# Kernel optimization log

Measured on AMD Instinct MI355X. Metric: run time of the kernel, lower is better.

Reference implementation:

```python
import jax, jax.numpy as jnp
import numpy as np

EPS = 1e-5
CIN = [3, 24, 48, 96, 192]
COUT = [24, 48, 96, 192, 384]
P = 512
NUM_CLASSES = 101
FC_IN = 384 * 16 * 3 * 3  # 55296


def _poly_layer(x, proj, alpha, gamma, beta):
    # x: (B, C, D, H, W)
    B, C, D, H, W = x.shape
    # im2col: 3x3x3 patches with zero padding 1 -> (B, C*27, D, H, W)
    patches = jax.lax.conv_general_dilated_patches(
        x, filter_shape=(3, 3, 3), window_strides=(1, 1, 1),
        padding=[(1, 1), (1, 1), (1, 1)])
    patches = jnp.moveaxis(patches, 1, -1)  # (B, D, H, W, C*27)
    ws = jnp.einsum('bdhwk,pk->bdhwp', patches, proj)      # projector GEMM
    out = jnp.einsum('bdhwp,po->bdhwo', ws, alpha)         # alpha GEMM
    out = jnp.maximum(1.0 + out, 0.0)                      # clamp(1+x, min=0)
    out = jnp.moveaxis(out, -1, 1)                         # (B, O, D, H, W)
    # MaxPool3d kernel/stride (1,2,2)
    out = jax.lax.reduce_window(out, -jnp.inf, jax.lax.max,
                                (1, 1, 1, 2, 2), (1, 1, 1, 2, 2), 'VALID')
    # BatchNorm3d with batch statistics (train-mode math)
    mean = out.mean(axis=(0, 2, 3, 4), keepdims=True)
    var = out.var(axis=(0, 2, 3, 4), keepdims=True)
    out = (out - mean) * jax.lax.rsqrt(var + EPS)
    out = out * gamma.reshape(1, -1, 1, 1, 1) + beta.reshape(1, -1, 1, 1, 1)
    return out


def setup_inputs() -> dict:
    key = jax.random.key(0)
    keys = jax.random.split(key, 32)
    inp = {'x': jax.random.normal(keys[0], (2, 3, 16, 112, 112), dtype=jnp.float32)}
    ki = 1
    for i in range(5):
        k_feat = CIN[i] * 27
        inp[f'p{i+1}'] = jax.random.normal(keys[ki], (P, k_feat), dtype=jnp.float32) / np.sqrt(k_feat); ki += 1
        inp[f'a{i+1}'] = jax.random.normal(keys[ki], (P, COUT[i]), dtype=jnp.float32) * np.sqrt(2.0 / COUT[i]); ki += 1
        inp[f'g{i+1}'] = jnp.ones((COUT[i],), dtype=jnp.float32)
        inp[f'q{i+1}'] = jnp.zeros((COUT[i],), dtype=jnp.float32)
    inp['w1'] = jax.random.normal(keys[ki], (512, FC_IN), dtype=jnp.float32) * np.sqrt(2.0 / 512); ki += 1
    inp['b1'] = jnp.zeros((512,), dtype=jnp.float32)
    inp['w2'] = jax.random.normal(keys[ki], (256, 512), dtype=jnp.float32) * np.sqrt(2.0 / 256); ki += 1
    inp['b2'] = jnp.zeros((256,), dtype=jnp.float32)
    inp['w3'] = jax.random.normal(keys[ki], (NUM_CLASSES, 256), dtype=jnp.float32) * np.sqrt(2.0 / NUM_CLASSES); ki += 1
    inp['b3'] = jnp.zeros((NUM_CLASSES,), dtype=jnp.float32)
    return inp


def reference(x, p1, a1, g1, q1, p2, a2, g2, q2, p3, a3, g3, q3,
              p4, a4, g4, q4, p5, a5, g5, q5, w1, b1, w2, b2, w3, b3):
    projs = [p1, p2, p3, p4, p5]
    alphas = [a1, a2, a3, a4, a5]
    gammas = [g1, g2, g3, g4, g5]
    betas = [q1, q2, q3, q4, q5]
    h = x
    for i in range(5):
        h = _poly_layer(h, projs[i], alphas[i], gammas[i], betas[i])
    h = h.reshape(h.shape[0], -1)  # (B, 55296)
    h = jax.nn.relu(h @ w1.T + b1)  # dropout = identity (eval)
    h = jax.nn.relu(h @ w2.T + b2)
    logits = h @ w3.T + b3
    return logits
```

## Files before the change

### kernel.cpp

```cpp
#include <hip/hip_runtime.h>

#define EPS_BN 1e-5f

typedef __attribute__((ext_vector_type(8))) short sh8;
typedef __attribute__((ext_vector_type(4))) short sh4;
typedef __attribute__((ext_vector_type(4))) float f32x4;

static const size_t PART_OFF = 2645784;
static const size_t PRE_OFF  = 6258456;
static const size_t OUT5_OFF = 8666904;
static const size_t H_OFF    = 8777496;
static const size_t ST_OFF   = 8888088;
static const size_t BNP_OFF  = 8888856;
static const size_t H1_OFF   = 8938008;
static const size_t WS_TOT   = 8939032;
__device__ __align__(256) float g_ws[WS_TOT];

static const size_t XIN_OFF = 0;
static const size_t A1_OFF  = 1871424;
static const size_t A2_OFF  = 4776768;
static const size_t A3_OFF  = 6331968;
static const size_t A4_OFF  = 7216704;
static const size_t AR_TOT  = 7776576;
__device__ __align__(256) unsigned short g_act[AR_TOT];

static const size_t WB_OFF[5] = {0, 4096, 36352, 162304, 659968};
static const size_t WB_TOT    = 2650624;
__device__ __align__(256) unsigned short g_wb[WB_TOT];

__device__ inline unsigned short f2bf(float v) {
    unsigned u = __float_as_uint(v);
    return (unsigned short)((u + 0x7fffu + ((u >> 16) & 1u)) >> 16);
}
__device__ inline float bf2f(unsigned short h) {
    return __uint_as_float(((unsigned)h) << 16);
}

__global__ __launch_bounds__(256) void init_input(const float* __restrict__ x,
                                                  unsigned short* __restrict__ xp,
                                                  float* __restrict__ bnp,
                                                  int4* __restrict__ zp, int nz,
                                                  int4* __restrict__ wbz, int nwb)
{
    const int i = blockIdx.x * 256 + threadIdx.x;
    if (i < nz) zp[i] = make_int4(0, 0, 0, 0);
    if (i < nwb) wbz[i] = make_int4(0, 0, 0, 0);
    if (i < 49152) bnp[i] = 0.f;
    if (i >= 2 * 18 * 114 * 114 * 4) return;
    const int c = i & 3;
    int t = i >> 2;
    const int xx = t % 114; t /= 114;
    const int yy = t % 114; t /= 114;
    const int zz = t % 18;
    const int b  = t / 18;
    float v = 0.f;
    if (c < 3 && (unsigned)(zz - 1) < 16u && (unsigned)(yy - 1) < 112u && (unsigned)(xx - 1) < 112u)
        v = x[(((size_t)b * 3 + c) * 16 + (zz - 1)) * 12544 + (yy - 1) * 112 + (xx - 1)];
    xp[i] = f2bf(v);
}

struct PrepArgs {
    const float* src[10];
    int W[10];
    int dstrow[10];
    int start[11];
    int rowtot;
};

__global__ __launch_bounds__(256) void prep_t(PrepArgs a, unsigned short* __restrict__ dst)
{
    __shared__ unsigned short tileh[32 * 72];
    __shared__ unsigned short tilel[32 * 72];
    int m = 0;
    {
        const int bx = blockIdx.x;
        while (m < 9 && bx >= a.start[m + 1]) ++m;
    }
    const int t  = blockIdx.x - a.start[m];
    const int tw = t >> 4, tp = t & 15;
    const int p0 = tp * 32, w0 = tw * 64;
    const int W = a.W[m];
    const float* __restrict__ src = a.src[m];
    const int tid = threadIdx.x;

    #pragma unroll
    for (int e = 0; e < 8; ++e) {
        const int idx = tid + e * 256;
        const int w = idx & 63, pr = idx >> 6;
        const int gw = w0 + w;
        float v = 0.f;
        if (gw < W) v = src[(size_t)(p0 + pr) * W + gw];
        const unsigned short hh = f2bf(v);
        tileh[pr * 72 + w] = hh;
        tilel[pr * 72 + w] = f2bf(v - bf2f(hh));
    }
    __syncthreads();
    {
        const int wr = tid >> 2, pg = (tid & 3) * 8;
        sh8 packh, packl;
        #pragma unroll
        for (int e = 0; e < 8; ++e) {
            packh[e] = (short)tileh[(pg + e) * 72 + wr];
            packl[e] = (short)tilel[(pg + e) * 72 + wr];
        }
        const size_t rh = (size_t)a.dstrow[m] + w0 + wr;
        *(sh8*)&dst[rh * 512 + p0 + pg] = packh;
        *(sh8*)&dst[(rh + a.rowtot) * 512 + p0 + pg] = packl;
    }
}

struct Fuse2Args {
    int aoff[5], poff[5];
    int wboff[5];
    int K[5], CO[5], KPAD[5], CPAD[5];
    int kt[5];
    int start[6];
    int rowtot;
};

__global__ __launch_bounds__(256) void fuse_mfma(const unsigned short* __restrict__ tb,
                                                 unsigned short* __restrict__ wb,
                                                 Fuse2Args a)
{
    int l = 0;
    {
        const int bx = blockIdx.x;
        while (l < 4 && bx >= a.start[l + 1]) ++l;
    }
    const int idx = blockIdx.x - a.start[l];
    const int ot = idx / a.kt[l];
    const int kt = idx % a.kt[l];
    const int lane = threadIdx.x & 63;
    const int wv = threadIdx.x >> 6;
    const size_t LOFF = (size_t)a.rowtot * 512;

    const unsigned short* arow = tb + ((size_t)(a.aoff[l] + ot * 64 + wv * 16 + (lane & 15))) * 512 + (lane >> 4) * 8;
    const unsigned short* brow = tb + ((size_t)(a.poff[l] + kt * 64 + (lane & 15))) * 512 + (lane >> 4) * 8;

    f32x4 acc[4];
    #pragma unroll
    for (int i = 0; i < 4; ++i) acc[i] = (f32x4){0.f, 0.f, 0.f, 0.f};

    #pragma unroll 2
    for (int p0 = 0; p0 < 512; p0 += 32) {
        const sh8 afh = *(const sh8*)(arow + p0);
        const sh8 afl = *(const sh8*)(arow + LOFF + p0);
        #pragma unroll
        for (int nt = 0; nt < 4; ++nt) {
            const sh8 bfh = *(const sh8*)(brow + (size_t)nt * 16 * 512 + p0);
            const sh8 bfl = *(const sh8*)(brow + LOFF + (size_t)nt * 16 * 512 + p0);
            acc[nt] = __builtin_amdgcn_mfma_f32_16x16x32_bf16(afh, bfh, acc[nt], 0, 0, 0);
            acc[nt] = __builtin_amdgcn_mfma_f32_16x16x32_bf16(afh, bfl, acc[nt], 0, 0, 0);
            acc[nt] = __builtin_amdgcn_mfma_f32_16x16x32_bf16(afl, bfh, acc[nt], 0, 0, 0);
        }
    }

    const int K = a.K[l], CO = a.CO[l], KP = a.KPAD[l], CP = a.CPAD[l];
    unsigned short* wbl = wb + a.wboff[l];
    #pragma unroll
    for (int nt = 0; nt < 4; ++nt) {
        const int kk = kt * 64 + nt * 16 + (lane & 15);
        if (kk < K) {
            const int c = kk / 27, s = kk - c * 27;
            const int col = s * CP + c;
            #pragma unroll
            for (int j = 0; j < 4; ++j) {
                const int o = ot * 64 + wv * 16 + (lane >> 4) * 4 + j;
                if (o < CO) wbl[(size_t)o * KP + col] = f2bf(acc[nt][j]);
            }
        }
    }
}

template<int CPAD, int COUT, int KPAD, int HI, int WI, int HP, int WP, int NBLK, int SPLIT>
__global__ __launch_bounds__(256) void conv_mfma(
    const unsigned short* __restrict__ in, const unsigned short* __restrict__ Wb,
    float* __restrict__ outf, float* __restrict__ part, float* __restrict__ bnp)
{
    constexpr int NT = NBLK / 16;
    constexpr int HI2 = HI + 2, WI2 = WI + 2;
    constexpr bool C8 = (CPAD % 8 == 0);
    constexpr int TABN = C8 ? KPAD / 8 : KPAD / 4;
    constexpr int NSTEP = KPAD / 32 / SPLIT;
    constexpr int MTOT = 2 * 16 * HP * WP * 4;
    constexpr bool BONCE = (NBLK * KPAD * 2 <= 16384);
    constexpr int BROW = BONCE ? (KPAD + 8) : 40;
    constexpr int BS_ELEMS = BONCE ? NBLK * BROW : 2 * NBLK * 40;

    __shared__ __align__(16) unsigned short As[2][128 * 40];
    __shared__ __align__(16) unsigned short Bs[BS_ELEMS];
    __shared__ int tab[TABN];
    __shared__ float bs[(SPLIT == 1) ? 2 * NBLK : 1];

    const int tid = threadIdx.x;
    const int lane = tid & 63;
    const int wv = tid >> 6;
    const int blk_m = blockIdx.x;
    const int oc0 = blockIdx.y * NBLK;
    const int kc = (SPLIT > 1) ? blockIdx.z : 0;

    for (int i = tid; i < TABN; i += 256) {
        const int k = i * (C8 ? 8 : 4);
        const int s = k / CPAD, c = k % CPAD;
        tab[i] = (s < 27) ? ((((s / 9) * HI2 + (s % 9) / 3) * WI2 + (s % 3)) * CPAD + c) : -1;
    }

    if constexpr (BONCE) {
        for (int i = tid; i < NBLK * KPAD / 8; i += 256) {
            const int r = i / (KPAD / 8), kk = i - r * (KPAD / 8);
            *(sh8*)&Bs[r * BROW + kk * 8] = *(const sh8*)&Wb[(size_t)(oc0 + r) * KPAD + kk * 8];
        }
    }

    const int srow = tid >> 1;
    const int half = tid & 1;
    const int m_g = blk_m * 128 + srow;
    const int pooled_s = m_g >> 2, sub_s = m_g & 3;
    const int pw_g = pooled_s % WP;
    const int ph_g = (pooled_s / WP) % HP;
    const int d_g  = (pooled_s / (WP * HP)) & 15;
    const int b_g  = pooled_s / (WP * HP * 16);
    const int h_g = 2 * ph_g + (sub_s >> 1);
    const int w_g = 2 * pw_g + (sub_s & 1);
    const size_t base_m = ((((size_t)b_g * 18 + d_g) * HI2 + h_g) * WI2 + w_g) * CPAD;

    const int brow = tid >> 2, bcc = tid & 3;
    const bool bload = (tid < NBLK * 4);

    f32x4 acc[2][NT];
    #pragma unroll
    for (int mf = 0; mf < 2; ++mf)
        #pragma unroll
        for (int i = 0; i < NT; ++i) acc[mf][i] = (f32x4){0.f, 0.f, 0.f, 0.f};

    const int k_begin = kc * NSTEP * 32;

    sh8 aA0, aA1;
    sh4 aP0, aP1, aP2, aP3;
    sh8 brg;

    __syncthreads();

    {
        const int k0 = k_begin;
        if constexpr (C8) {
            const int o0 = tab[(k0 >> 3) + half * 2];
            const int o1 = tab[(k0 >> 3) + half * 2 + 1];
            aA0 = (sh8){0, 0, 0, 0, 0, 0, 0, 0};
            aA1 = (sh8){0, 0, 0, 0, 0, 0, 0, 0};
            if (o0 >= 0) aA0 = *(const sh8*)(in + base_m + o0);
            if (o1 >= 0) aA1 = *(const sh8*)(in + base_m + o1);
            *(sh8*)&As[0][srow * 40 + (half * 2) * 8]     = aA0;
            *(sh8*)&As[0][srow * 40 + (half * 2 + 1) * 8] = aA1;
        } else {
            const int t0 = tab[(k0 >> 2) + half * 4];
            const int t1 = tab[(k0 >> 2) + half * 4 + 1];
            const int t2 = tab[(k0 >> 2) + half * 4 + 2];
            const int t3 = tab[(k0 >> 2) + half * 4 + 3];
            aP0 = (sh4){0, 0, 0, 0}; aP1 = (sh4){0, 0, 0, 0};
            aP2 = (sh4){0, 0, 0, 0}; aP3 = (sh4){0, 0, 0, 0};
            if (t0 >= 0) aP0 = *(const sh4*)(in + base_m + t0);
            if (t1 >= 0) aP1 = *(const sh4*)(in + base_m + t1);
            if (t2 >= 0) aP2 = *(const sh4*)(in + base_m + t2);
            if (t3 >= 0) aP3 = *(const sh4*)(in + base_m + t3);
            *(sh4*)&As[0][srow * 40 + (half * 4) * 4]     = aP0;
            *(sh4*)&As[0][srow * 40 + (half * 4 + 1) * 4] = aP1;
            *(sh4*)&As[0][srow * 40 + (half * 4 + 2) * 4] = aP2;
            *(sh4*)&As[0][srow * 40 + (half * 4 + 3) * 4] = aP3;
        }
        if constexpr (!BONCE) {
            if (bload) {
                brg = *(const sh8*)&Wb[(size_t)(oc0 + brow) * KPAD + k0 + bcc * 8];
                *(sh8*)&Bs[0 + brow * 40 + bcc * 8] = brg;
            }
        }
    }
    __syncthreads();

    int cur = 0;
    for (int s = 0; s < NSTEP; ++s) {
        const int k0 = k_begin + s * 32;
        if (s + 1 < NSTEP) {
            const int kn = k0 + 32;
            if constexpr (C8) {
                const int o0 = tab[(kn >> 3) + half * 2];
                const int o1 = tab[(kn >> 3) + half * 2 + 1];
                aA0 = (sh8){0, 0, 0, 0, 0, 0, 0, 0};
                aA1 = (sh8){0, 0, 0, 0, 0, 0, 0, 0};
                if (o0 >= 0) aA0 = *(const sh8*)(in + base_m + o0);
                if (o1 >= 0) aA1 = *(const sh8*)(in + base_m + o1);
            } else {
                const int t0 = tab[(kn >> 2) + half * 4];
                const int t1 = tab[(kn >> 2) + half * 4 + 1];
                const int t2 = tab[(kn >> 2) + half * 4 + 2];
                const int t3 = tab[(kn >> 2) + half * 4 + 3];
                aP0 = (sh4){0, 0, 0, 0}; aP1 = (sh4){0, 0, 0, 0};
                aP2 = (sh4){0, 0, 0, 0}; aP3 = (sh4){0, 0, 0, 0};
                if (t0 >= 0) aP0 = *(const sh4*)(in + base_m + t0);
                if (t1 >= 0) aP1 = *(const sh4*)(in + base_m + t1);
                if (t2 >= 0) aP2 = *(const sh4*)(in + base_m + t2);
                if (t3 >= 0) aP3 = *(const sh4*)(in + base_m + t3);
            }
            if constexpr (!BONCE) {
                if (bload) brg = *(const sh8*)&Wb[(size_t)(oc0 + brow) * KPAD + kn + bcc * 8];
            }
        }
        const sh8 af0 = *(const sh8*)&As[cur][(wv * 16 + (lane & 15)) * 40 + (lane >> 4) * 8];
        const sh8 af1 = *(const sh8*)&As[cur][(64 + wv * 16 + (lane & 15)) * 40 + (lane >> 4) * 8];
        #pragma unroll
        for (int nt = 0; nt < NT; ++nt) {
            sh8 bf;
            if constexpr (BONCE)
                bf = *(const sh8*)&Bs[(nt * 16 + (lane & 15)) * BROW + k0 + (lane >> 4) * 8];
            else
                bf = *(const sh8*)&Bs[cur * NBLK * 40 + (nt * 16 + (lane & 15)) * 40 + (lane >> 4) * 8];
            acc[0][nt] = __builtin_amdgcn_mfma_f32_16x16x32_bf16(af0, bf, acc[0][nt], 0, 0, 0);
            acc[1][nt] = __builtin_amdgcn_mfma_f32_16x16x32_bf16(af1, bf, acc[1][nt], 0, 0, 0);
        }
        if (s + 1 < NSTEP) {
            if constexpr (C8) {
                *(sh8*)&As[cur ^ 1][srow * 40 + (half * 2) * 8]     = aA0;
                *(sh8*)&As[cur ^ 1][srow * 40 + (half * 2 + 1) * 8] = aA1;
            } else {
                *(sh4*)&As[cur ^ 1][srow * 40 + (half * 4) * 4]     = aP0;
                *(sh4*)&As[cur ^ 1][srow * 40 + (half * 4 + 1) * 4] = aP1;
                *(sh4*)&As[cur ^ 1][srow * 40 + (half * 4 + 2) * 4] = aP2;
                *(sh4*)&As[cur ^ 1][srow * 40 + (half * 4 + 3) * 4] = aP3;
            }
            if constexpr (!BONCE) {
                if (bload) *(sh8*)&Bs[(cur ^ 1) * NBLK * 40 + brow * 40 + bcc * 8] = brg;
            }
        }
        __syncthreads();
        cur ^= 1;
    }

    const int q = lane >> 4;
    const int nloc = lane & 15;
    if constexpr (SPLIT == 1) {
        for (int i = tid; i < 2 * NBLK; i += 256) bs[i] = 0.f;
        __syncthreads();
        #pragma unroll
        for (int mf = 0; mf < 2; ++mf) {
            const int pooled_o = blk_m * 32 + mf * 16 + wv * 4 + q;
            #pragma unroll
            for (int nt = 0; nt < NT; ++nt) {
                const int oc = oc0 + nt * 16 + nloc;
                float mx = fmaxf(1.f + acc[mf][nt][0], 0.f);
                mx = fmaxf(mx, fmaxf(1.f + acc[mf][nt][1], 0.f));
                mx = fmaxf(mx, fmaxf(1.f + acc[mf][nt][2], 0.f));
                mx = fmaxf(mx, fmaxf(1.f + acc[mf][nt][3], 0.f));
                float s1 = 0.f;
                if (oc < COUT) {
                    outf[(size_t)pooled_o * COUT + oc] = mx;
                    s1 = mx;
                }
                float s2 = s1 * s1;
                s1 += __shfl_xor(s1, 16);
                s1 += __shfl_xor(s1, 32);
                s2 += __shfl_xor(s2, 16);
                s2 += __shfl_xor(s2, 32);
                if (q == 0) {
                    atomicAdd(&bs[nt * 16 + nloc], s1);
                    atomicAdd(&bs[NBLK + nt * 16 + nloc], s2);
                }
            }
        }
        __syncthreads();
        float* rowp = bnp + (size_t)(blk_m & 63) * 768;
        for (int i = tid; i < NBLK; i += 256) {
            const int oc = oc0 + i;
            if (oc < COUT) {
                atomicAdd(&rowp[oc], bs[i]);
                atomicAdd(&rowp[384 + oc], bs[NBLK + i]);
            }
        }
    } else {
        #pragma unroll
        for (int mf = 0; mf < 2; ++mf) {
            #pragma unroll
            for (int nt = 0; nt < NT; ++nt) {
                const int oc = oc0 + nt * 16 + nloc;
                #pragma unroll
                for (int r = 0; r < 4; ++r) {
                    const int mm = blk_m * 128 + mf * 64 + wv * 16 + q * 4 + r;
                    part[((size_t)kc * MTOT + mm) * COUT + oc] = acc[mf][nt][r];
                }
            }
        }
    }
}

template<int COUT, int HP, int WP, int SPLIT>
__global__ __launch_bounds__(256) void pool_epi(const float* __restrict__ part,
                                                float* __restrict__ outf,
                                                float* __restrict__ bnp)
{
    constexpr int PO = 2 * 16 * HP * WP;
    constexpr int M = PO * 4;
    __shared__ float bs[2 * COUT];
    const int tid = threadIdx.x;
    for (int i = tid; i < 2 * COUT; i += 256) bs[i] = 0.f;
    __syncthreads();
    const int idx = blockIdx.x * 256 + tid;
    if (idx < PO * COUT) {
        const int oc = idx % COUT;
        const int p = idx / COUT;
        float v[4] = {0.f, 0.f, 0.f, 0.f};
        for (int s = 0; s < SPLIT; ++s)
            #pragma unroll
            for (int r = 0; r < 4; ++r)
                v[r] += part[((size_t)s * M + p * 4 + r) * COUT + oc];
        float mx = fmaxf(1.f + v[0], 0.f);
        mx = fmaxf(mx, fmaxf(1.f + v[1], 0.f));
        mx = fmaxf(mx, fmaxf(1.f + v[2], 0.f));
        mx = fmaxf(mx, fmaxf(1.f + v[3], 0.f));
        outf[(size_t)p * COUT + oc] = mx;
        atomicAdd(&bs[oc], mx);
        atomicAdd(&bs[COUT + oc], mx * mx);
    }
    __syncthreads();
    float* rowp = bnp + (size_t)(blockIdx.x & 63) * 768;
    for (int i = tid; i < COUT; i += 256) {
        atomicAdd(&rowp[i], bs[i]);
        atomicAdd(&rowp[384 + i], bs[COUT + i]);
    }
}

__global__ __launch_bounds__(64) void bn_reduce(float* __restrict__ bnp,
                                                const float* __restrict__ gamma,
                                                const float* __restrict__ beta,
                                                float* __restrict__ st,
                                                float inv_n)
{
    const int c = blockIdx.x, tid = threadIdx.x;
    float s = bnp[(size_t)tid * 768 + c];
    float q = bnp[(size_t)tid * 768 + 384 + c];
    bnp[(size_t)tid * 768 + c] = 0.f;
    bnp[(size_t)tid * 768 + 384 + c] = 0.f;
    #pragma unroll
    for (int off = 32; off > 0; off >>= 1) {
        s += __shfl_down(s, off);
        q += __shfl_down(q, off);
    }
    if (tid == 0) {
        const float mean = s * inv_n;
        const float var  = q * inv_n - mean * mean;
        const float sc   = gamma[c] * rsqrtf(var + EPS_BN);
        st[2 * c]     = sc;
        st[2 * c + 1] = fmaf(-mean, sc, beta[c]);
    }
}

template<int C, int HP, int WP>
__global__ __launch_bounds__(256) void bn_apply_halo(const float* __restrict__ pre,
                                                     const float* __restrict__ st,
                                                     unsigned short* __restrict__ outh)
{
    constexpr int PO = 2 * 16 * HP * WP;
    const int idx = blockIdx.x * 256 + threadIdx.x;
    if (idx >= PO * C) return;
    const int c = idx % C;
    const int p = idx / C;
    const int pw = p % WP;
    const int ph = (p / WP) % HP;
    const int d  = (p / (WP * HP)) & 15;
    const int b  = p / (WP * HP * 16);
    const float v = fmaf(pre[idx], st[2 * c], st[2 * c + 1]);
    outh[((((size_t)b * 18 + d + 1) * (HP + 2) + ph + 1) * (WP + 2) + pw + 1) * C + c] = f2bf(v);
}

__global__ __launch_bounds__(256) void transpose5(const float* __restrict__ out5,
                                                  const float* __restrict__ st,
                                                  float* __restrict__ h)
{
    const int idx = blockIdx.x * 256 + threadIdx.x;
    if (idx >= 110592) return;
    const int c = idx % 384;
    const int p = idx / 384;
    const int b = p / 144;
    const int sp = p % 144;
    h[(size_t)b * 55296 + c * 144 + sp] = fmaf(out5[idx], st[2 * c], st[2 * c + 1]);
}

__global__ __launch_bounds__(256) void fc1_k(const float* __restrict__ h,
                                             const float* __restrict__ w1,
                                             const float* __restrict__ b1,
                                             float* __restrict__ hout)
{
    __shared__ float r0[256];
    __shared__ float r1[256];
    const int j = blockIdx.x, tid = threadIdx.x;
    const float* wr = w1 + (size_t)j * 55296;
    float a0 = 0.f, a1 = 0.f;
    for (int k = tid * 4; k < 55296; k += 1024) {
        const float4 w = *(const float4*)(wr + k);
        const float4 u = *(const float4*)(h + k);
        const float4 v = *(const float4*)(h + 55296 + k);
        a0 += w.x * u.x + w.y * u.y + w.z * u.z + w.w * u.w;
        a1 += w.x * v.x + w.y * v.y + w.z * v.z + w.w * v.w;
    }
    r0[tid] = a0; r1[tid] = a1;
    __syncthreads();
    for (int off = 128; off > 0; off >>= 1) {
        if (tid < off) { r0[tid] += r0[tid + off]; r1[tid] += r1[tid + off]; }
        __syncthreads();
    }
    if (tid == 0) {
        hout[j]       = fmaxf(r0[0] + b1[j], 0.f);
        hout[512 + j] = fmaxf(r1[0] + b1[j], 0.f);
    }
}

__global__ __launch_bounds__(256) void fc23_k(const float* __restrict__ h1,
                                              const float* __restrict__ w2,
                                              const float* __restrict__ b2,
                                              const float* __restrict__ w3,
                                              const float* __restrict__ b3,
                                              float* __restrict__ out)
{
    __shared__ float h1s[1024];
    __shared__ float h2[512];
    const int tid = threadIdx.x;
    for (int i = tid; i < 1024; i += 256) h1s[i] = h1[i];
    __syncthreads();
    {
        const float* wr = w2 + (size_t)tid * 512;
        #pragma unroll
        for (int b = 0; b < 2; ++b) {
            float a = 0.f;
            const float* hh = h1s + b * 512;
            for (int k = 0; k < 512; ++k) a = fmaf(wr[k], hh[k], a);
            h2[b * 256 + tid] = fmaxf(a + b2[tid], 0.f);
        }
    }
    __syncthreads();
    if (tid < 101) {
        const float* wr = w3 + (size_t)tid * 256;
        #pragma unroll
        for (int b = 0; b < 2; ++b) {
            float a = 0.f;
            const float* hh = h2 + b * 256;
            for (int k = 0; k < 256; ++k) a = fmaf(wr[k], hh[k], a);
            out[b * 101 + tid] = a + b3[tid];
        }
    }
}

extern "C" void kernel_launch(void* const* d_in, const int* in_sizes, int n_in,
                              void* d_out, int out_size, void* d_ws, size_t ws_size,
                              hipStream_t stream)
{
    const float* x  = (const float*)d_in[0];
    const float* p[5], *al[5], *g[5], *q[5];
    for (int i = 0; i < 5; ++i) {
        p[i]  = (const float*)d_in[1 + 4 * i];
        al[i] = (const float*)d_in[2 + 4 * i];
        g[i]  = (const float*)d_in[3 + 4 * i];
        q[i]  = (const float*)d_in[4 + 4 * i];
    }
    const float* w1 = (const float*)d_in[21];
    const float* b1 = (const float*)d_in[22];
    const float* w2 = (const float*)d_in[23];
    const float* b2 = (const float*)d_in[24];
    const float* w3 = (const float*)d_in[25];
    const float* b3 = (const float*)d_in[26];

    float* ws = nullptr;
    hipGetSymbolAddress((void**)&ws, HIP_SYMBOL(g_ws));
    unsigned short* act = nullptr;
    hipGetSymbolAddress((void**)&act, HIP_SYMBOL(g_act));
    unsigned short* wb = nullptr;
    hipGetSymbolAddress((void**)&wb, HIP_SYMBOL(g_wb));

    float* part = ws + PART_OFF;
    float* pre  = ws + PRE_OFF;
    float* out5 = ws + OUT5_OFF;
    float* h    = ws + H_OFF;
    float* st   = ws + ST_OFF;
    float* bnp  = ws + BNP_OFF;
    float* h1   = ws + H1_OFF;
    unsigned short* tbuf = (unsigned short*)(ws + PART_OFF);

    unsigned short* xin = act + XIN_OFF;
    unsigned short* a1  = act + A1_OFF;
    unsigned short* a2  = act + A2_OFF;
    unsigned short* a3  = act + A3_OFF;
    unsigned short* a4  = act + A4_OFF;

    static const int KF[5] = {81, 648, 1296, 2592, 5184};
    static const int CO[5] = {24, 48, 96, 192, 384};
    static const int CP[5] = {4, 24, 48, 96, 192};
    static const int KP[5] = {128, 672, 1312, 2592, 5184};
    static const int APAD[5] = {64, 64, 128, 192, 384};
    static const int PPAD[5] = {128, 704, 1344, 2624, 5184};
    static const int KT[5] = {2, 11, 21, 41, 81};
    static const int OT[5] = {1, 1, 2, 3, 6};

    {
        const int nz = (int)((AR_TOT - A1_OFF) * 2 / 16);
        const int nwb = (int)(WB_TOT * 2 / 16);
        init_input<<<(2 * 18 * 114 * 114 * 4 + 255) / 256, 256, 0, stream>>>(
            x, xin, bnp, (int4*)(act + A1_OFF), nz, (int4*)wb, nwb);
    }

    PrepArgs pa;
    Fuse2Args f2;
    int rowtot = 0;
    {
        int row = 0, blk = 0;
        pa.start[0] = 0;
        for (int i = 0; i < 5; ++i) {
            pa.src[i] = al[i]; pa.W[i] = CO[i]; pa.dstrow[i] = row;
            f2.aoff[i] = row;
            row += APAD[i];
            blk += (APAD[i] / 64) * 16;
            pa.start[i + 1] = blk;
        }
        for (int i = 0; i < 5; ++i) {
            pa.src[5 + i] = p[i]; pa.W[5 + i] = KF[i]; pa.dstrow[5 + i] = row;
            f2.poff[i] = row;
            row += PPAD[i];
            blk += (PPAD[i] / 64) * 16;
            pa.start[5 + i + 1] = blk;
        }
        rowtot = row;
        pa.rowtot = rowtot;
        f2.rowtot = rowtot;
        prep_t<<<blk, 256, 0, stream>>>(pa, tbuf);
    }

    {
        int s0 = 0;
        for (int i = 0; i < 5; ++i) {
            f2.wboff[i] = (int)WB_OFF[i];
            f2.K[i] = KF[i]; f2.CO[i] = CO[i]; f2.KPAD[i] = KP[i]; f2.CPAD[i] = CP[i];
            f2.kt[i] = KT[i];
            f2.start[i] = s0;
            s0 += KT[i] * OT[i];
        }
        f2.start[5] = s0;
        fuse_mfma<<<s0, 256, 0, stream>>>(tbuf, wb, f2);
    }

    conv_mfma<4, 24, 128, 112, 112, 56, 56, 32, 1>
        <<<dim3(3136, 1), 256, 0, stream>>>(xin, wb + WB_OFF[0], pre, nullptr, bnp);
    bn_reduce<<<24, 64, 0, stream>>>(bnp, g[0], q[0], st, 1.f / 100352.f);
    bn_apply_halo<24, 56, 56><<<9408, 256, 0, stream>>>(pre, st, a1);

    conv_mfma<24, 48, 672, 56, 56, 28, 28, 48, 1>
        <<<dim3(784, 1), 256, 0, stream>>>(a1, wb + WB_OFF[1], pre, nullptr, bnp);
    bn_reduce<<<48, 64, 0, stream>>>(bnp, g[1], q[1], st, 1.f / 25088.f);
    bn_apply_halo<48, 28, 28><<<4704, 256, 0, stream>>>(pre, st, a2);

    conv_mfma<48, 96, 1312, 28, 28, 14, 14, 48, 1>
        <<<dim3(196, 2), 256, 0, stream>>>(a2, wb + WB_OFF[2], pre, nullptr, bnp);
    bn_reduce<<<96, 64, 0, stream>>>(bnp, g[2], q[2], st, 1.f / 6272.f);
    bn_apply_halo<96, 14, 14><<<2352, 256, 0, stream>>>(pre, st, a3);

    conv_mfma<96, 192, 2592, 14, 14, 7, 7, 64, 3>
        <<<dim3(49, 3, 3), 256, 0, stream>>>(a3, wb + WB_OFF[3], nullptr, part, bnp);
    pool_epi<192, 7, 7, 3><<<1176, 256, 0, stream>>>(part, pre, bnp);
    bn_reduce<<<192, 64, 0, stream>>>(bnp, g[3], q[3], st, 1.f / 1568.f);
    bn_apply_halo<192, 7, 7><<<1176, 256, 0, stream>>>(pre, st, a4);

    conv_mfma<192, 384, 5184, 7, 7, 3, 3, 64, 6>
        <<<dim3(9, 6, 6), 256, 0, stream>>>(a4, wb + WB_OFF[4], nullptr, part, bnp);
    pool_epi<384, 3, 3, 6><<<432, 256, 0, stream>>>(part, out5, bnp);
    bn_reduce<<<384, 64, 0, stream>>>(bnp, g[4], q[4], st, 1.f / 288.f);

    transpose5<<<(110592 + 255) / 256, 256, 0, stream>>>(out5, st, h);
    fc1_k<<<512, 256, 0, stream>>>(h, w1, b1, h1);
    fc23_k<<<1, 256, 0, stream>>>(h1, w2, b2, w3, b3, (float*)d_out);
}
```

Measured before the change: 542.4 us.

## Restructure weight-fusion GEMM to cover all output tiles per block, add reorder pass

```diff
diff --git a/kernel.cpp b/kernel.cpp
--- a/kernel.cpp
+++ b/kernel.cpp
@@ -109,67 +109,111 @@
     }
 }
 
-struct Fuse2Args {
+struct Fuse3Args {
     int aoff[5], poff[5];
-    int wboff[5];
-    int K[5], CO[5], KPAD[5], CPAD[5];
-    int kt[5];
+    int woff[5];
+    int KL[5];
+    int noft[5];
     int start[6];
     int rowtot;
 };
 
 __global__ __launch_bounds__(256) void fuse_mfma(const unsigned short* __restrict__ tb,
-                                                 unsigned short* __restrict__ wb,
-                                                 Fuse2Args a)
+                                                 unsigned short* __restrict__ wlin,
+                                                 Fuse3Args a)
 {
     int l = 0;
     {
         const int bx = blockIdx.x;
         while (l < 4 && bx >= a.start[l + 1]) ++l;
     }
-    const int idx = blockIdx.x - a.start[l];
-    const int ot = idx / a.kt[l];
-    const int kt = idx % a.kt[l];
+    const int kt = blockIdx.x - a.start[l];
     const int lane = threadIdx.x & 63;
     const int wv = threadIdx.x >> 6;
     const size_t LOFF = (size_t)a.rowtot * 512;
-
-    const unsigned short* arow = tb + ((size_t)(a.aoff[l] + ot * 64 + wv * 16 + (lane & 15))) * 512 + (lane >> 4) * 8;
-    const unsigned short* brow = tb + ((size_t)(a.poff[l] + kt * 64 + (lane & 15))) * 512 + (lane >> 4) * 8;
-
-    f32x4 acc[4];
+    const int noft = a.noft[l];
+
+    const unsigned short* bbase = tb + ((size_t)(a.poff[l] + kt * 64 + (lane & 15))) * 512 + (lane >> 4) * 8;
+    const unsigned short* abase = tb + ((size_t)(a.aoff[l] + (lane & 15))) * 512 + (lane >> 4) * 8;
+
+    f32x4 acc[6][4];
     #pragma unroll
-    for (int i = 0; i < 4; ++i) acc[i] = (f32x4){0.f, 0.f, 0.f, 0.f};
-
-    #pragma unroll 2
+    for (int of = 0; of < 6; ++of)
+        #pragma unroll
+        for (int nt = 0; nt < 4; ++nt) acc[of][nt] = (f32x4){0.f, 0.f, 0.f, 0.f};
+
     for (int p0 = 0; p0 < 512; p0 += 32) {
-        const sh8 afh = *(const sh8*)(arow + p0);
-        const sh8 afl = *(const sh8*)(arow + LOFF + p0);
+        sh8 bh[4], bl[4];
         #pragma unroll
         for (int nt = 0; nt < 4; ++nt) {
-            const sh8 bfh = *(const sh8*)(brow + (size_t)nt * 16 * 512 + p0);
-            const sh8 bfl = *(const sh8*)(brow + LOFF + (size_t)nt * 16 * 512 + p0);
-            acc[nt] = __builtin_amdgcn_mfma_f32_16x16x32_bf16(afh, bfh, acc[nt], 0, 0, 0);
-            acc[nt] = __builtin_amdgcn_mfma_f32_16x16x32_bf16(afh, bfl, acc[nt], 0, 0, 0);
-            acc[nt] = __builtin_amdgcn_mfma_f32_16x16x32_bf16(afl, bfh, acc[nt], 0, 0, 0);
-        }
-    }
-
-    const int K = a.K[l], CO = a.CO[l], KP = a.KPAD[l], CP = a.CPAD[l];
-    unsigned short* wbl = wb + a.wboff[l];
+            bh[nt] = *(const sh8*)(bbase + (size_t)nt * 16 * 512 + p0);
+            bl[nt] = *(const sh8*)(bbase + LOFF + (size_t)nt * 16 * 512 + p0);
+        }
+        #pragma unroll
+        for (int of = 0; of < 6; ++of) {
+            const int f = of * 4 + wv;
+            if (f < noft) {
+                const sh8 ah = *(const sh8*)(abase + (size_t)f * 16 * 512 + p0);
+                const sh8 alo = *(const sh8*)(abase + LOFF + (size_t)f * 16 * 512 + p0);
+                #pragma unroll
+                for (int nt = 0; nt < 4; ++nt) {
+                    acc[of][nt] = __builtin_amdgcn_mfma_f32_16x16x32_bf16(ah, bh[nt], acc[of][nt], 0, 0, 0);
+                    acc[of][nt] = __builtin_amdgcn_mfma_f32_16x16x32_bf16(ah, bl[nt], acc[of][nt], 0, 0, 0);
+                    acc[of][nt] = __builtin_amdgcn_mfma_f32_16x16x32_bf16(alo, bh[nt], acc[of][nt], 0, 0, 0);
+                }
+            }
+        }
+    }
+
+    const int KL = a.KL[l];
+    unsigned short* wrow = wlin + a.woff[l];
     #pragma unroll
-    for (int nt = 0; nt < 4; ++nt) {
-        const int kk = kt * 64 + nt * 16 + (lane & 15);
-        if (kk < K) {
-            const int c = kk / 27, s = kk - c * 27;
-            const int col = s * CP + c;
+    for (int of = 0; of < 6; ++of) {
+        const int f = of * 4 + wv;
+        if (f < noft) {
             #pragma unroll
-            for (int j = 0; j < 4; ++j) {
-                const int o = ot * 64 + wv * 16 + (lane >> 4) * 4 + j;
-                if (o < CO) wbl[(size_t)o * KP + col] = f2bf(acc[nt][j]);
-            }
-        }
-    }
+            for (int nt = 0; nt < 4; ++nt) {
+                const int k = kt * 64 + nt * 16 + (lane & 15);
+                #pragma unroll
+                for (int j = 0; j < 4; ++j) {
+                    const int o = f * 16 + (lane >> 4) * 4 + j;
+                    wrow[(size_t)o * KL + k] = f2bf(acc[of][nt][j]);
+                }
+            }
+        }
+    }
+}
+
+struct ReordBArgs {
+    int woff[5], wboff[5];
+    int K[5], KL[5], KP[5], CP[5];
+    int start[6];
+};
+
+__global__ __launch_bounds__(256) void reorder_b(const unsigned short* __restrict__ wlin,
+                                                 unsigned short* __restrict__ wb,
+                                                 ReordBArgs a)
+{
+    __shared__ __align__(16) unsigned short lds[5184];
+    int l = 0;
+    {
+        const int bx = blockIdx.x;
+        while (l < 4 && bx >= a.start[l + 1]) ++l;
+    }
+    const int o = blockIdx.x - a.start[l];
+    const int K = a.K[l], KL = a.KL[l], KP = a.KP[l], CP = a.CP[l];
+    const int tid = threadIdx.x;
+    for (int i = tid; i < KP; i += 256) lds[i] = 0;
+    __syncthreads();
+    const unsigned short* src = wlin + a.woff[l] + (size_t)o * KL;
+    for (int k = tid; k < K; k += 256) {
+        const int c = k / 27, s = k - c * 27;
+        lds[s * CP + c] = src[k];
+    }
+    __syncthreads();
+    unsigned short* drow = wb + a.wboff[l] + (size_t)o * KP;
+    for (int i = tid * 8; i < KP; i += 2048)
+        *(sh8*)&drow[i] = *(const sh8*)&lds[i];
 }
 
 template<int CPAD, int COUT, int KPAD, int HI, int WI, int HP, int WP, int NBLK, int SPLIT>
@@ -580,7 +624,8 @@
     float* st   = ws + ST_OFF;
     float* bnp  = ws + BNP_OFF;
     float* h1   = ws + H1_OFF;
-    unsigned short* tbuf = (unsigned short*)(ws + PART_OFF);
+    unsigned short* tbuf = (unsigned short*)ws;
+    unsigned short* wlin = tbuf + (size_t)2 * 10816 * 512;
 
     unsigned short* xin = act + XIN_OFF;
     unsigned short* a1  = act + A1_OFF;
@@ -595,7 +640,8 @@
     static const int APAD[5] = {64, 64, 128, 192, 384};
     static const int PPAD[5] = {128, 704, 1344, 2624, 5184};
     static const int KT[5] = {2, 11, 21, 41, 81};
-    static const int OT[5] = {1, 1, 2, 3, 6};
+    static const int NOFT[5] = {2, 3, 6, 12, 24};
+    static const int NPAD[5] = {32, 48, 96, 192, 384};
 
     {
         const int nz = (int)((AR_TOT - A1_OFF) * 2 / 16);
@@ -605,42 +651,56 @@
     }
 
     PrepArgs pa;
-    Fuse2Args f2;
-    int rowtot = 0;
+    Fuse3Args f3;
+    ReordBArgs rb;
     {
         int row = 0, blk = 0;
         pa.start[0] = 0;
         for (int i = 0; i < 5; ++i) {
             pa.src[i] = al[i]; pa.W[i] = CO[i]; pa.dstrow[i] = row;
-            f2.aoff[i] = row;
+            f3.aoff[i] = row;
             row += APAD[i];
             blk += (APAD[i] / 64) * 16;
             pa.start[i + 1] = blk;
         }
         for (int i = 0; i < 5; ++i) {
             pa.src[5 + i] = p[i]; pa.W[5 + i] = KF[i]; pa.dstrow[5 + i] = row;
-            f2.poff[i] = row;
+            f3.poff[i] = row;
             row += PPAD[i];
             blk += (PPAD[i] / 64) * 16;
             pa.start[5 + i + 1] = blk;
         }
-        rowtot = row;
-        pa.rowtot = rowtot;
-        f2.rowtot = rowtot;
+        pa.rowtot = row;
+        f3.rowtot = row;
         prep_t<<<blk, 256, 0, stream>>>(pa, tbuf);
     }
 
     {
-        int s0 = 0;
+        int s0 = 0, woff = 0;
         for (int i = 0; i < 5; ++i) {
-            f2.wboff[i] = (int)WB_OFF[i];
-            f2.K[i] = KF[i]; f2.CO[i] = CO[i]; f2.KPAD[i] = KP[i]; f2.CPAD[i] = CP[i];
-            f2.kt[i] = KT[i];
-            f2.start[i] = s0;
-            s0 += KT[i] * OT[i];
-        }
-        f2.start[5] = s0;
-        fuse_mfma<<<s0, 256, 0, stream>>>(tbuf, wb, f2);
+            f3.woff[i] = woff;
+            f3.KL[i] = KT[i] * 64;
+            f3.noft[i] = NOFT[i];
+            f3.start[i] = s0;
+            s0 += KT[i];
+            woff += NPAD[i] * KT[i] * 64;
+        }
+        f3.start[5] = s0;
+        fuse_mfma<<<s0, 256, 0, stream>>>(tbuf, wlin, f3);
+    }
+
+    {
+        int s0 = 0, woff = 0;
+        for (int i = 0; i < 5; ++i) {
+            rb.woff[i] = woff;
+            rb.wboff[i] = (int)WB_OFF[i];
+            rb.K[i] = KF[i]; rb.KL[i] = KT[i] * 64; rb.KP[i] = KP[i]; rb.CP[i] = CP[i];
+            rb.start[i] = s0;
+            s0 += CO[i];
+            woff += NPAD[i] * KT[i] * 64;
+        }
+        rb.start[5] = s0;
+        reorder_b<<<s0, 256, 0, stream>>>(wlin, wb, rb);
     }
 
     conv_mfma<4, 24, 128, 112, 112, 56, 56, 32, 1>
```

Result: no change. 540.4 us (-0.4%).
